# Optimization experiments

Measured on AMD Instinct MI355X. Metric: run time of the kernel, lower is better.

Reference implementation:

```python
import jax, jax.numpy as jnp
import numpy as np

RADIUS = 5
KERNEL_SIZE = 2 * RADIUS - 1  # 9
PAD = KERNEL_SIZE // 2        # 4
H, W = 2048, 2048


def make_distance_kernel():
    center = RADIUS - 1
    y, x = jnp.meshgrid(jnp.arange(KERNEL_SIZE), jnp.arange(KERNEL_SIZE), indexing='ij')
    d = jnp.sqrt((x - center).astype(jnp.float32) ** 2 + (y - center).astype(jnp.float32) ** 2)
    return d.at[center, center].set(0.0)


def setup_inputs() -> dict:
    key = jax.random.key(0)
    target = (jax.random.uniform(key, (5, H, W)) < 0.15).astype(jnp.float32)
    distance_kernel = make_distance_kernel()
    return {"target": target, "distance_kernel": distance_kernel}


def _contour_weights(target, kernel):
    combined = (target.sum(axis=0) > 0).astype(jnp.float32)          # [H, W]
    padded = jnp.pad(combined, PAD, mode='edge')                      # replicate pad
    min_d = jnp.full_like(combined, jnp.inf)
    inf = jnp.float32(jnp.inf)
    for i in range(KERNEL_SIZE):
        for j in range(KERNEL_SIZE):
            if i == PAD and j == PAD:
                continue
            shifted = padded[i:i + H, j:j + W]
            diff = (shifted != combined).astype(jnp.float32)
            dist = jnp.where(diff > 0, kernel[i, j] / (diff + 1e-10), inf)
            min_d = jnp.minimum(min_d, dist)
    return jnp.where(min_d < inf, 1.0 / (min_d + 1e-10), 0.0)


def reference(target, distance_kernel):
    feature_weight = target.sum(axis=0)                               # [H, W]
    contour = _contour_weights(target, distance_kernel)
    weights = (feature_weight + contour) ** 2
    weights = (weights - weights.min()) / (weights.max() - weights.min() + 1e-10)
    return weights * (target.sum(axis=0) > 0).astype(jnp.float32)
```

## Files before the change

kernel.cpp:

```cpp
#include <hip/hip_runtime.h>
#include <hip/hip_fp16.h>
#include <stdint.h>

#define HH 2048
#define WW 2048
#define NPIX (HH*WW)
#define MROW (WW/32)
#define TSX 64
#define TSY 32
#define NBLK ((WW/TSX)*(HH/TSY))

__global__ __launch_bounds__(256) void fw_kernel(
    const float* __restrict__ target, uint8_t* __restrict__ fw,
    uint32_t* __restrict__ mask)
{
    __shared__ uint8_t nib[256];
    const int t = threadIdx.x;
    const int i = blockIdx.x * 256 + t;
    const float4* t4 = (const float4*)target;
    float4 a = t4[i];
    float4 b = t4[(NPIX/4) + i];
    float4 c = t4[2*(NPIX/4) + i];
    float4 d = t4[3*(NPIX/4) + i];
    float4 e = t4[4*(NPIX/4) + i];
    uchar4 o;
    o.x = (unsigned char)(a.x + b.x + c.x + d.x + e.x);
    o.y = (unsigned char)(a.y + b.y + c.y + d.y + e.y);
    o.z = (unsigned char)(a.z + b.z + c.z + d.z + e.z);
    o.w = (unsigned char)(a.w + b.w + c.w + d.w + e.w);
    ((uchar4*)fw)[i] = o;
    nib[t] = (uint8_t)((o.x ? 1u : 0u) | (o.y ? 2u : 0u) | (o.z ? 4u : 0u) | (o.w ? 8u : 0u));
    __syncthreads();
    if (t < 32) {
        const uint8_t* p = nib + t * 8;
        uint32_t w = 0;
        #pragma unroll
        for (int k = 0; k < 8; ++k) w |= (uint32_t)p[k] << (4 * k);
        mask[blockIdx.x * 32 + t] = w;
    }
}

__global__ __launch_bounds__(256) void contour_kernel(
    const uint8_t* __restrict__ fw, const uint32_t* __restrict__ mask,
    const float* __restrict__ dk,
    __half* __restrict__ wh, float* __restrict__ pmin, float* __restrict__ pmax)
{
    __shared__ uint32_t maskw[TSY + 8][4];
    __shared__ float inv_d2[40];
    __shared__ float redmn[4], redmx[4];

    const int t   = threadIdx.x;
    const int gx0 = blockIdx.x * TSX;
    const int gy0 = blockIdx.y * TSY;

    if (t < 81) {
        int iy = t / 9, jx = t - (t / 9) * 9;
        int dy = iy - 4, dx = jx - 4;
        int d2 = dy * dy + dx * dx;
        if (d2 != 0)
            inv_d2[d2] = 1.0f / (dk[t] / (1.0f + 1e-10f) + 1e-10f);
    }

    const int w0 = gx0 >> 5;
    if (t < (TSY + 8) * 4) {
        int hr = t >> 2, wc = t & 3;
        int gy = gy0 - 4 + hr; gy = min(max(gy, 0), HH - 1);
        const uint32_t* rowp = mask + gy * MROW;
        int wi = w0 - 1 + wc;
        uint32_t v;
        if (wi < 0)            v = (rowp[0] & 1u) ? 0xFFFFFFFFu : 0u;
        else if (wi > MROW-1)  v = (rowp[MROW-1] >> 31) ? 0xFFFFFFFFu : 0u;
        else                   v = rowp[wi];
        maskw[hr][wc] = v;
    }
    __syncthreads();

    const int tx   = t & 63;
    const int wid  = t >> 6;
    const int r0   = wid * 8;
    const int pos  = tx + 28;
    const int wsel = pos >> 5;
    const uint32_t sh = (uint32_t)(pos & 31);
    const int gx = gx0 + tx;

    float fwv[8];
    #pragma unroll
    for (int r = 0; r < 8; ++r)
        fwv[r] = (float)fw[(gy0 + r0 + r) * WW + gx];

    uint32_t w9[9];
    #pragma unroll
    for (int k = 0; k < 9; ++k) {
        uint32_t lo = maskw[r0 + k][wsel];
        uint32_t hi = maskw[r0 + k][wsel + 1];
        w9[k] = (uint32_t)(((((uint64_t)hi) << 32) | lo) >> sh) & 0x1FFu;
    }

    float lmn = __int_as_float(0x7F800000);
    float lmx = 0.0f;

    #pragma unroll
    for (int r = 0; r < 8; ++r) {
        uint32_t cbit = (w9[4] >> 4) & 1u;
        uint32_t cm = 0u - cbit;
        uint32_t mind2 = 999u;
        #pragma unroll
        for (int dy = 0; dy < 9; ++dy) {
            uint32_t x = (w9[dy] ^ cm) & 0x1FFu;
            uint32_t rev = __builtin_bitreverse32(x) >> 23;
            uint32_t g = (((x | rev) >> 4) & 0x1Fu) | 0x100u;
            uint32_t mk = (uint32_t)__builtin_ctz(g);
            uint32_t d2 = mk * mk + (uint32_t)((dy - 4) * (dy - 4));
            mind2 = min(mind2, d2);
        }
        float contour = (mind2 <= 32u) ? inv_d2[mind2] : 0.0f;
        float wv = fwv[r] + contour;
        wv = wv * wv;
        __half h = __float2half(wv);
        wh[(gy0 + r0 + r) * WW + gx] = h;
        float wr = __half2float(h);
        lmn = fminf(lmn, wr);
        lmx = fmaxf(lmx, wr);
        if (r < 7) {
            #pragma unroll
            for (int k = 0; k < 8; ++k) w9[k] = w9[k + 1];
            uint32_t lo = maskw[r0 + r + 9][wsel];
            uint32_t hi = maskw[r0 + r + 9][wsel + 1];
            w9[8] = (uint32_t)(((((uint64_t)hi) << 32) | lo) >> sh) & 0x1FFu;
        }
    }

    #pragma unroll
    for (int off = 32; off > 0; off >>= 1) {
        lmn = fminf(lmn, __shfl_xor(lmn, off));
        lmx = fmaxf(lmx, __shfl_xor(lmx, off));
    }
    if (tx == 0) { redmn[wid] = lmn; redmx[wid] = lmx; }
    __syncthreads();
    if (t == 0) {
        float mn = fminf(fminf(redmn[0], redmn[1]), fminf(redmn[2], redmn[3]));
        float mx = fmaxf(fmaxf(redmx[0], redmx[1]), fmaxf(redmx[2], redmx[3]));
        int bid = blockIdx.y * gridDim.x + blockIdx.x;
        pmin[bid] = mn;
        pmax[bid] = mx;
    }
}

__global__ __launch_bounds__(256) void norm_kernel(
    const __half* __restrict__ wh, const uint32_t* __restrict__ mask,
    const float* __restrict__ pmin, const float* __restrict__ pmax,
    float* __restrict__ out)
{
    __shared__ float smn[4], smx[4];
    const int t = threadIdx.x;

    const float4* pn4 = (const float4*)pmin;
    const float4* px4 = (const float4*)pmax;
    float4 a = pn4[t * 2], b = pn4[t * 2 + 1];
    float4 c = px4[t * 2], d = px4[t * 2 + 1];
    float mn = fminf(fminf(fminf(a.x, a.y), fminf(a.z, a.w)),
                     fminf(fminf(b.x, b.y), fminf(b.z, b.w)));
    float mx = fmaxf(fmaxf(fmaxf(c.x, c.y), fmaxf(c.z, c.w)),
                     fmaxf(fmaxf(d.x, d.y), fmaxf(d.z, d.w)));
    #pragma unroll
    for (int off = 32; off > 0; off >>= 1) {
        mn = fminf(mn, __shfl_xor(mn, off));
        mx = fmaxf(mx, __shfl_xor(mx, off));
    }
    if ((t & 63) == 0) { smn[t >> 6] = mn; smx[t >> 6] = mx; }
    __syncthreads();
    mn = fminf(fminf(smn[0], smn[1]), fminf(smn[2], smn[3]));
    mx = fmaxf(fmaxf(smx[0], smx[1]), fmaxf(smx[2], smx[3]));
    const float rden = 1.0f / (mx - mn + 1e-10f);

    const int i = blockIdx.x * 256 + t;
    float4 v = ((const float4*)wh)[i];
    const __half2* hp = (const __half2*)&v;
    uint32_t mb = (mask[i >> 2] >> ((i & 3) * 8)) & 0xFFu;
    float2 f0 = __half22float2(hp[0]);
    float2 f1 = __half22float2(hp[1]);
    float2 f2 = __half22float2(hp[2]);
    float2 f3 = __half22float2(hp[3]);
    float4 o0, o1;
    o0.x = (mb &   1u) ? (f0.x - mn) * rden : 0.0f;
    o0.y = (mb &   2u) ? (f0.y - mn) * rden : 0.0f;
    o0.z = (mb &   4u) ? (f1.x - mn) * rden : 0.0f;
    o0.w = (mb &   8u) ? (f1.y - mn) * rden : 0.0f;
    o1.x = (mb &  16u) ? (f2.x - mn) * rden : 0.0f;
    o1.y = (mb &  32u) ? (f2.y - mn) * rden : 0.0f;
    o1.z = (mb &  64u) ? (f3.x - mn) * rden : 0.0f;
    o1.w = (mb & 128u) ? (f3.y - mn) * rden : 0.0f;
    ((float4*)out)[i * 2]     = o0;
    ((float4*)out)[i * 2 + 1] = o1;
}

extern "C" void kernel_launch(void* const* d_in, const int* in_sizes, int n_in,
                              void* d_out, int out_size, void* d_ws, size_t ws_size,
                              hipStream_t stream)
{
    const float* target = (const float*)d_in[0];
    const float* dk     = (const float*)d_in[1];
    float* out = (float*)d_out;

    uint8_t* wsb = (uint8_t*)d_ws;
    uint8_t*  fw   = wsb;
    uint32_t* mask = (uint32_t*)(wsb + NPIX);
    __half*   wh   = (__half*)(wsb + NPIX + NPIX/8);
    float*    pmin = (float*)(wsb + NPIX + NPIX/8 + 2*NPIX);
    float*    pmax = pmin + NBLK;

    fw_kernel<<<NPIX / 4 / 256, 256, 0, stream>>>(target, fw, mask);

    dim3 gridB(WW / TSX, HH / TSY);
    contour_kernel<<<gridB, 256, 0, stream>>>(fw, mask, dk, wh, pmin, pmax);

    norm_kernel<<<NPIX / 8 / 256, 256, 0, stream>>>(wh, mask, pmin, pmax, out);
}
```

Baseline: 39.43 us.

## Encode per-pixel weight as one-byte code and decode via LUT in normalize

The contour kernel now writes an 8-bit code per pixel (squared contour distance index plus feature count) in place of an fp16 weight, and the normalize kernel rebuilds the weight from a 256-entry shared LUT. The normalize kernel also takes the foreground test from the code instead of reading the bitmask. Per-pixel intermediate traffic drops from 2 bytes plus a mask read to 1 byte. Inside the contour kernel, each thread now handles 8 horizontal pixels of one row, symmetric row pairs are pre-combined with OR/AND, and a shared LUT replaces the bitreverse/ctz distance computation. The trade-off is added LUT setup and extra syncs in every block, and the exact weights avoid fp16 rounding.

```diff
diff --git a/kernel.cpp b/kernel.cpp
--- a/kernel.cpp
+++ b/kernel.cpp
@@ -1,5 +1,4 @@
 #include <hip/hip_runtime.h>
-#include <hip/hip_fp16.h>
 #include <stdint.h>
 
 #define HH 2048
@@ -43,24 +42,24 @@
 __global__ __launch_bounds__(256) void contour_kernel(
     const uint8_t* __restrict__ fw, const uint32_t* __restrict__ mask,
     const float* __restrict__ dk,
-    __half* __restrict__ wh, float* __restrict__ pmin, float* __restrict__ pmax)
+    uint8_t* __restrict__ wcode, float* __restrict__ pmin, float* __restrict__ pmax)
 {
     __shared__ uint32_t maskw[TSY + 8][4];
-    __shared__ float inv_d2[40];
-    __shared__ float redmn[4], redmx[4];
+    __shared__ uint8_t  lutm2[512];
+    __shared__ float    inv_ext[101];
+    __shared__ float    redmn[4], redmx[4];
 
     const int t   = threadIdx.x;
     const int gx0 = blockIdx.x * TSX;
     const int gy0 = blockIdx.y * TSY;
 
-    if (t < 81) {
-        int iy = t / 9, jx = t - (t / 9) * 9;
-        int dy = iy - 4, dx = jx - 4;
-        int d2 = dy * dy + dx * dx;
-        if (d2 != 0)
-            inv_d2[d2] = 1.0f / (dk[t] / (1.0f + 1e-10f) + 1e-10f);
-    }
-
+    if (t < 101) inv_ext[t] = 0.0f;
+    for (int idx = t; idx < 512; idx += 256) {
+        uint32_t rev = __builtin_bitreverse32((uint32_t)idx) >> 23;
+        uint32_t g = ((((uint32_t)idx | rev) >> 4) & 0x1Fu) | 0x100u;
+        uint32_t mk = (uint32_t)__builtin_ctz(g);
+        lutm2[idx] = (uint8_t)(mk * mk);
+    }
     const int w0 = gx0 >> 5;
     if (t < (TSY + 8) * 4) {
         int hr = t >> 2, wc = t & 3;
@@ -74,68 +73,76 @@
         maskw[hr][wc] = v;
     }
     __syncthreads();
-
-    const int tx   = t & 63;
-    const int wid  = t >> 6;
-    const int r0   = wid * 8;
-    const int pos  = tx + 28;
+    if (t < 81) {
+        int iy = t / 9, jx = t - (t / 9) * 9;
+        int dy = iy - 4, dx = jx - 4;
+        int d2 = dy * dy + dx * dx;
+        if (d2 != 0)
+            inv_ext[d2] = 1.0f / (dk[t] / (1.0f + 1e-10f) + 1e-10f);
+    }
+    __syncthreads();
+
+    const int rl  = t >> 3;
+    const int xg  = t & 7;
+    const int gy  = gy0 + rl;
+    const int gxb = gx0 + xg * 8;
+
+    uint32_t fwlo = *(const uint32_t*)(fw + gy * WW + gxb);
+    uint32_t fwhi = *(const uint32_t*)(fw + gy * WW + gxb + 4);
+
+    const int pos  = xg * 8 + 28;
     const int wsel = pos >> 5;
     const uint32_t sh = (uint32_t)(pos & 31);
-    const int gx = gx0 + tx;
-
-    float fwv[8];
-    #pragma unroll
-    for (int r = 0; r < 8; ++r)
-        fwv[r] = (float)fw[(gy0 + r0 + r) * WW + gx];
-
-    uint32_t w9[9];
+    uint32_t wrow[9];
     #pragma unroll
     for (int k = 0; k < 9; ++k) {
-        uint32_t lo = maskw[r0 + k][wsel];
-        uint32_t hi = maskw[r0 + k][wsel + 1];
-        w9[k] = (uint32_t)(((((uint64_t)hi) << 32) | lo) >> sh) & 0x1FFu;
+        uint64_t v = (((uint64_t)maskw[rl + k][wsel + 1]) << 32) | maskw[rl + k][wsel];
+        wrow[k] = (uint32_t)(v >> sh);
+    }
+    uint32_t orx[4], andx[4];
+    #pragma unroll
+    for (int k = 1; k <= 4; ++k) {
+        orx[k-1]  = wrow[4 - k] | wrow[4 + k];
+        andx[k-1] = wrow[4 - k] & wrow[4 + k];
     }
 
     float lmn = __int_as_float(0x7F800000);
     float lmx = 0.0f;
-
-    #pragma unroll
-    for (int r = 0; r < 8; ++r) {
-        uint32_t cbit = (w9[4] >> 4) & 1u;
-        uint32_t cm = 0u - cbit;
-        uint32_t mind2 = 999u;
+    uint32_t outb0 = 0, outb1 = 0;
+
+    #pragma unroll
+    for (int j = 0; j < 8; ++j) {
+        uint32_t craw = (wrow[4] >> (4 + j)) & 1u;
+        uint32_t cm = 0u - craw;
+        uint32_t x0 = ((wrow[4] ^ cm) >> j) & 0x1FFu;
+        uint32_t d2m = (uint32_t)lutm2[x0];
         #pragma unroll
-        for (int dy = 0; dy < 9; ++dy) {
-            uint32_t x = (w9[dy] ^ cm) & 0x1FFu;
-            uint32_t rev = __builtin_bitreverse32(x) >> 23;
-            uint32_t g = (((x | rev) >> 4) & 0x1Fu) | 0x100u;
-            uint32_t mk = (uint32_t)__builtin_ctz(g);
-            uint32_t d2 = mk * mk + (uint32_t)((dy - 4) * (dy - 4));
-            mind2 = min(mind2, d2);
+        for (int k = 1; k <= 4; ++k) {
+            uint32_t sel = craw ? andx[k-1] : orx[k-1];
+            uint32_t x = ((sel ^ cm) >> j) & 0x1FFu;
+            uint32_t d2 = (uint32_t)lutm2[x] + (uint32_t)(k * k);
+            d2m = min(d2m, d2);
         }
-        float contour = (mind2 <= 32u) ? inv_d2[mind2] : 0.0f;
-        float wv = fwv[r] + contour;
+        float contour = inv_ext[d2m];
+        uint32_t enc = (d2m > 32u) ? 26u : d2m;
+        uint32_t fwj = (j < 4 ? (fwlo >> (8 * j)) : (fwhi >> (8 * (j - 4)))) & 0xFFu;
+        uint32_t code = ((enc - 1u) << 3) | fwj;
+        if (j < 4) outb0 |= code << (8 * j);
+        else       outb1 |= code << (8 * (j - 4));
+        float wv = (float)fwj + contour;
         wv = wv * wv;
-        __half h = __float2half(wv);
-        wh[(gy0 + r0 + r) * WW + gx] = h;
-        float wr = __half2float(h);
-        lmn = fminf(lmn, wr);
-        lmx = fmaxf(lmx, wr);
-        if (r < 7) {
-            #pragma unroll
-            for (int k = 0; k < 8; ++k) w9[k] = w9[k + 1];
-            uint32_t lo = maskw[r0 + r + 9][wsel];
-            uint32_t hi = maskw[r0 + r + 9][wsel + 1];
-            w9[8] = (uint32_t)(((((uint64_t)hi) << 32) | lo) >> sh) & 0x1FFu;
-        }
-    }
+        lmn = fminf(lmn, wv);
+        lmx = fmaxf(lmx, wv);
+    }
+    uint2 ob; ob.x = outb0; ob.y = outb1;
+    *(uint2*)(wcode + gy * WW + gxb) = ob;
 
     #pragma unroll
     for (int off = 32; off > 0; off >>= 1) {
         lmn = fminf(lmn, __shfl_xor(lmn, off));
         lmx = fmaxf(lmx, __shfl_xor(lmx, off));
     }
-    if (tx == 0) { redmn[wid] = lmn; redmx[wid] = lmx; }
+    if ((t & 63) == 0) { redmn[t >> 6] = lmn; redmx[t >> 6] = lmx; }
     __syncthreads();
     if (t == 0) {
         float mn = fminf(fminf(redmn[0], redmn[1]), fminf(redmn[2], redmn[3]));
@@ -147,17 +154,32 @@
 }
 
 __global__ __launch_bounds__(256) void norm_kernel(
-    const __half* __restrict__ wh, const uint32_t* __restrict__ mask,
+    const uint8_t* __restrict__ wcode, const float* __restrict__ dk,
     const float* __restrict__ pmin, const float* __restrict__ pmax,
     float* __restrict__ out)
 {
+    __shared__ float ct[33];
+    __shared__ float wlut[256];
     __shared__ float smn[4], smx[4];
     const int t = threadIdx.x;
 
+    if (t < 33) ct[t] = 0.0f;
     const float4* pn4 = (const float4*)pmin;
     const float4* px4 = (const float4*)pmax;
     float4 a = pn4[t * 2], b = pn4[t * 2 + 1];
     float4 c = px4[t * 2], d = px4[t * 2 + 1];
+    __syncthreads();
+    if (t < 81) {
+        int iy = t / 9, jx = t - (t / 9) * 9;
+        int dy = iy - 4, dx = jx - 4;
+        int d2 = dy * dy + dx * dx;
+        if (d2 != 0) ct[d2] = 1.0f / (dk[t] / (1.0f + 1e-10f) + 1e-10f);
+    }
+    __syncthreads();
+    {
+        float wv = (float)(t & 7) + ct[(t >> 3) + 1];
+        wlut[t] = wv * wv;
+    }
     float mn = fminf(fminf(fminf(a.x, a.y), fminf(a.z, a.w)),
                      fminf(fminf(b.x, b.y), fminf(b.z, b.w)));
     float mx = fmaxf(fmaxf(fmaxf(c.x, c.y), fmaxf(c.z, c.w)),
@@ -174,22 +196,17 @@
     const float rden = 1.0f / (mx - mn + 1e-10f);
 
     const int i = blockIdx.x * 256 + t;
-    float4 v = ((const float4*)wh)[i];
-    const __half2* hp = (const __half2*)&v;
-    uint32_t mb = (mask[i >> 2] >> ((i & 3) * 8)) & 0xFFu;
-    float2 f0 = __half22float2(hp[0]);
-    float2 f1 = __half22float2(hp[1]);
-    float2 f2 = __half22float2(hp[2]);
-    float2 f3 = __half22float2(hp[3]);
+    uint2 cb = ((const uint2*)wcode)[i];
+    uint32_t b0 = cb.x, b1 = cb.y;
     float4 o0, o1;
-    o0.x = (mb &   1u) ? (f0.x - mn) * rden : 0.0f;
-    o0.y = (mb &   2u) ? (f0.y - mn) * rden : 0.0f;
-    o0.z = (mb &   4u) ? (f1.x - mn) * rden : 0.0f;
-    o0.w = (mb &   8u) ? (f1.y - mn) * rden : 0.0f;
-    o1.x = (mb &  16u) ? (f2.x - mn) * rden : 0.0f;
-    o1.y = (mb &  32u) ? (f2.y - mn) * rden : 0.0f;
-    o1.z = (mb &  64u) ? (f3.x - mn) * rden : 0.0f;
-    o1.w = (mb & 128u) ? (f3.y - mn) * rden : 0.0f;
+    o0.x = (b0 & 7u)         ? (wlut[b0 & 0xFFu] - mn) * rden         : 0.0f;
+    o0.y = ((b0 >> 8) & 7u)  ? (wlut[(b0 >> 8) & 0xFFu] - mn) * rden  : 0.0f;
+    o0.z = ((b0 >> 16) & 7u) ? (wlut[(b0 >> 16) & 0xFFu] - mn) * rden : 0.0f;
+    o0.w = ((b0 >> 24) & 7u) ? (wlut[b0 >> 24] - mn) * rden           : 0.0f;
+    o1.x = (b1 & 7u)         ? (wlut[b1 & 0xFFu] - mn) * rden         : 0.0f;
+    o1.y = ((b1 >> 8) & 7u)  ? (wlut[(b1 >> 8) & 0xFFu] - mn) * rden  : 0.0f;
+    o1.z = ((b1 >> 16) & 7u) ? (wlut[(b1 >> 16) & 0xFFu] - mn) * rden : 0.0f;
+    o1.w = ((b1 >> 24) & 7u) ? (wlut[b1 >> 24] - mn) * rden           : 0.0f;
     ((float4*)out)[i * 2]     = o0;
     ((float4*)out)[i * 2 + 1] = o1;
 }
@@ -203,16 +220,16 @@
     float* out = (float*)d_out;
 
     uint8_t* wsb = (uint8_t*)d_ws;
-    uint8_t*  fw   = wsb;
-    uint32_t* mask = (uint32_t*)(wsb + NPIX);
-    __half*   wh   = (__half*)(wsb + NPIX + NPIX/8);
-    float*    pmin = (float*)(wsb + NPIX + NPIX/8 + 2*NPIX);
-    float*    pmax = pmin + NBLK;
+    uint8_t*  fw    = wsb;
+    uint8_t*  wcode = wsb + NPIX;
+    uint32_t* mask  = (uint32_t*)(wsb + 2 * NPIX);
+    float*    pmin  = (float*)(wsb + 2 * NPIX + NPIX / 8);
+    float*    pmax  = pmin + NBLK;
 
     fw_kernel<<<NPIX / 4 / 256, 256, 0, stream>>>(target, fw, mask);
 
     dim3 gridB(WW / TSX, HH / TSY);
-    contour_kernel<<<gridB, 256, 0, stream>>>(fw, mask, dk, wh, pmin, pmax);
-
-    norm_kernel<<<NPIX / 8 / 256, 256, 0, stream>>>(wh, mask, pmin, pmax, out);
-}
+    contour_kernel<<<gridB, 256, 0, stream>>>(fw, mask, dk, wcode, pmin, pmax);
+
+    norm_kernel<<<NPIX / 8 / 256, 256, 0, stream>>>(wcode, dk, pmin, pmax, out);
+}
```

Measured after the change: 35.09 us. 11.0% less time.
